# Performance work log

Measured on AMD Instinct MI355X. Metric: run time of the kernel, lower is better.

Reference implementation:

```python
import jax, jax.numpy as jnp
import numpy as np

TAU_PRE = 2.0
TAU_POST = 2.0


def setup_inputs() -> dict:
    key = jax.random.key(0)
    k1, k2, k3 = jax.random.split(key, 3)
    T, B, PRE, POST = 64, 16, 4096, 4096
    in_spikes = jax.random.uniform(k1, (T, B, PRE), dtype=jnp.float32)
    out_spikes = jax.random.uniform(k2, (T, B, POST), dtype=jnp.float32)
    weight = jax.random.normal(k3, (POST, PRE), dtype=jnp.float32)
    return {"in_spikes": in_spikes, "out_spikes": out_spikes, "weight": weight}


def reference(in_spikes, out_spikes, weight):
    # in_spikes: [T, B, pre]; out_spikes: [T, B, post]; weight: [post, pre]
    T, B, PRE = in_spikes.shape
    POST = out_spikes.shape[-1]

    def step(carry, xs):
        trace_pre, trace_post, delta_w = carry
        i_sp, o_sp = xs
        trace_pre = jnp.clip(trace_pre - trace_pre / TAU_PRE + i_sp, 0.0, 1.0)  # [B, pre]
        trace_post = trace_post - trace_post / TAU_POST + o_sp  # [B, post]
        # sum_b o[b,post]*trace_pre[b,pre] - (sum_b o[b,post]*trace_post[b,post]) * w[post,pre]
        dw = (jnp.einsum('bo,bp->op', o_sp, trace_pre)
              - (o_sp * trace_post).sum(0)[:, None] * weight)
        return (trace_pre, trace_post, delta_w + dw), None

    init = (jnp.zeros((B, PRE), in_spikes.dtype),
            jnp.zeros((B, POST), out_spikes.dtype),
            jnp.zeros((POST, PRE), weight.dtype))
    (trace_pre, trace_post, delta_w), _ = jax.lax.scan(step, init, (in_spikes, out_spikes))
    return delta_w
```

## Files before the change

### kernel.cpp

```cpp
#include <hip/hip_runtime.h>


#define T_STEPS 64
#define B_SZ    16
#define PRE     4096
#define POST    4096
#define K_TOT   1024

typedef __attribute__((ext_vector_type(8))) unsigned short ushort8;
typedef __attribute__((ext_vector_type(8))) __bf16 bf16x8;
typedef __attribute__((ext_vector_type(4))) float floatx4;

__device__ __forceinline__ unsigned short f2bf(float f) {
    unsigned int u = __float_as_uint(f);
    u += 0x7fff + ((u >> 16) & 1);
    return (unsigned short)(u >> 16);
}

__device__ __forceinline__ void glds16(const void* g, void* l) {
    __builtin_amdgcn_global_load_lds((const __attribute__((address_space(1))) void*)g,
                                     (__attribute__((address_space(3))) void*)l,
                                     16, 0, 0);
}

__global__ __launch_bounds__(256) void trace_convert(
        const float* __restrict__ in_spikes,
        const float* __restrict__ out_spikes,
        unsigned short* __restrict__ AT,
        unsigned short* __restrict__ BT,
        float* __restrict__ coef) {
    __shared__ float ldsf[4096];
    __shared__ unsigned short ot[128 * 34];
    __shared__ float cbuf[8][33];
    const int tid  = threadIdx.x;
    const int wave = tid >> 6;
    const int lane = tid & 63;
    const bool isA = blockIdx.x >= 128;
    const int p0 = (blockIdx.x & 127) * 32;
    const float* src = isA ? out_spikes : in_spikes;
    unsigned short* dst = isA ? AT : BT;

    const int bA = tid >> 5;
    const int pA = tid & 31;

    float st0 = 0.f, st1 = 0.f, c0 = 0.f, c1 = 0.f;

    for (int tc = 0; tc < 8; ++tc) {
        const int T0 = tc * 8;
        #pragma unroll
        for (int i = 0; i < 4; ++i) {
            const int q  = (wave * 4 + i) * 64 + lane;
            const int p  = (q & 7) * 4;
            const int b  = (q >> 3) & 15;
            const int tl = q >> 7;
            const float* g = src + ((size_t)((T0 + tl) * 16 + b)) * 4096 + p0 + p;
            glds16(g, (char*)ldsf + (size_t)(wave * 4 + i) * 1024);
        }
        __syncthreads();

        #pragma unroll
        for (int tl = 0; tl < 8; ++tl) {
            const float x0 = ldsf[tl * 512 + bA * 32 + pA];
            const float x1 = ldsf[tl * 512 + (bA + 8) * 32 + pA];
            if (isA) {
                st0 = 0.5f * st0 + x0; c0 += x0 * st0;
                st1 = 0.5f * st1 + x1; c1 += x1 * st1;
                ot[(tl * 16 + bA)     * 34 + pA] = f2bf(x0);
                ot[(tl * 16 + bA + 8) * 34 + pA] = f2bf(x1);
            } else {
                st0 = fminf(fmaxf(0.5f * st0 + x0, 0.f), 1.f);
                st1 = fminf(fmaxf(0.5f * st1 + x1, 0.f), 1.f);
                ot[(tl * 16 + bA)     * 34 + pA] = f2bf(st0);
                ot[(tl * 16 + bA + 8) * 34 + pA] = f2bf(st1);
            }
        }
        __syncthreads();

        const int pf = tid >> 3;
        const int c8 = tid & 7;
        #pragma unroll
        for (int i = 0; i < 2; ++i) {
            const int ch = c8 + i * 8;
            ushort8 v;
            #pragma unroll
            for (int s = 0; s < 8; ++s) v[s] = ot[(ch * 8 + s) * 34 + pf];
            *(ushort8*)&dst[(size_t)(p0 + pf) * K_TOT + T0 * 16 + ch * 8] = v;
        }
    }

    if (isA) {
        cbuf[bA][pA] = c0 + c1;
        __syncthreads();
        if (tid < 32) {
            float s = 0.f;
            #pragma unroll
            for (int r = 0; r < 8; ++r) s += cbuf[r][tid];
            coef[p0 + tid] = s;
        }
    }
}

#define NTILES 16

#define LOFF(buf, isB, kh) ((buf) * 65536 + (isB) * 32768 + (kh) * 16384)

__global__ __launch_bounds__(512, 2) void stdp_gemm_mfma(
        const unsigned short* __restrict__ AT,
        const unsigned short* __restrict__ BT,
        const float* __restrict__ W,
        const float* __restrict__ coef,
        float* __restrict__ Cout) {
    __shared__ __align__(16) char ldsraw[131072];

    const int tid  = threadIdx.x;
    const int lane = tid & 63;
    const int wave = tid >> 6;

    const int bid = blockIdx.x;
    const int f   = (bid & 7) * 32 + (bid >> 3);
    const int m0  = (f >> 4) * 256;
    const int n0  = (f & 15) * 256;

    const int wm  = (wave >> 2) * 128;
    const int wn  = (wave & 3) * 64;
    const int rml = lane & 15;
    const int q   = lane >> 4;
    const int swz16 = ((q ^ ((rml >> 1) & 3)) << 4);

    floatx4 acc[8][4];
    #pragma unroll
    for (int i = 0; i < 8; ++i)
        #pragma unroll
        for (int j = 0; j < 4; ++j)
            acc[i][j] = (floatx4){0.f, 0.f, 0.f, 0.f};
    bf16x8 bv[4];

    const int cid0 = wave * 64 + lane;
    const int row0 = cid0 >> 2;
    const int g0   = (cid0 & 3) ^ ((row0 >> 1) & 3);
    const unsigned short* gA0 = AT + (size_t)(m0 + row0) * K_TOT + g0 * 8;
    const unsigned short* gB0 = BT + (size_t)(n0 + row0) * K_TOT + g0 * 8;

    #define STG(isB, t, kh)                                                        \
        do {                                                                       \
            const unsigned short* s0_ = ((isB) ? gB0 : gA0) + (t) * 64 + (kh) * 32;\
            char* d_ = ldsraw + LOFF((t) & 1, (isB), (kh)) + wave * 1024;          \
            glds16(s0_, d_);                                                       \
            glds16(s0_ + (size_t)128 * K_TOT, d_ + 8192);                          \
        } while (0)

    #define PHASE(bufc, khc, mqc, SISB, ST, SKH, SCOND, WM)                        \
        do {                                                                       \
            const char* Ab_ = ldsraw + LOFF(bufc, 0, khc);                         \
            const char* Bb_ = ldsraw + LOFF(bufc, 1, khc);                         \
            if ((mqc) == 0) {                                                      \
                _Pragma("unroll")                                                  \
                for (int ni = 0; ni < 4; ++ni)                                     \
                    bv[ni] = *(const bf16x8*)(Bb_ + (wn + ni * 16 + rml) * 64 + swz16); \
            }                                                                      \
            bf16x8 af_[4];                                                         \
            _Pragma("unroll")                                                      \
            for (int k4 = 0; k4 < 4; ++k4)                                         \
                af_[k4] = *(const bf16x8*)(Ab_ + (wm + (mqc) * 64 + k4 * 16 + rml) * 64 + swz16); \
            if (SCOND) STG(SISB, ST, SKH);                                         \
            if ((WM) == 1)      asm volatile("s_waitcnt vmcnt(4)" ::: "memory");   \
            else if ((WM) == 2) asm volatile("s_waitcnt vmcnt(0)" ::: "memory");   \
            __builtin_amdgcn_s_barrier();                                          \
            __builtin_amdgcn_sched_barrier(0);                                     \
            __builtin_amdgcn_s_setprio(1);                                         \
            _Pragma("unroll")                                                      \
            for (int k4 = 0; k4 < 4; ++k4)                                         \
                _Pragma("unroll")                                                  \
                for (int ni = 0; ni < 4; ++ni)                                     \
                    acc[(mqc) * 4 + k4][ni] = __builtin_amdgcn_mfma_f32_16x16x32_bf16( \
                        af_[k4], bv[ni], acc[(mqc) * 4 + k4][ni], 0, 0, 0);        \
            __builtin_amdgcn_s_setprio(0);                                         \
            __builtin_amdgcn_s_barrier();                                          \
            __builtin_amdgcn_sched_barrier(0);                                     \
        } while (0)

    STG(0, 0, 0); STG(1, 0, 0); STG(0, 0, 1); STG(1, 0, 1);
    STG(0, 1, 0); STG(1, 1, 0); STG(0, 1, 1); STG(1, 1, 1);
    asm volatile("s_waitcnt vmcnt(8)" ::: "memory");
    __builtin_amdgcn_s_barrier();
    __builtin_amdgcn_sched_barrier(0);

    for (int i = 0; i < 8; ++i) {
        const int t2 = 2 * i + 2, t3 = 2 * i + 3, tA = 2 * i + 1;
        const int wm4 = (i < 7) ? 1 : 2;
        const int wm8 = (i < 7) ? 1 : 0;
        PHASE(0, 0, 0, 0, tA, 1, i > 0,      0);
        PHASE(0, 0, 1, 1, tA, 1, i > 0,      0);
        PHASE(0, 1, 0, 0, t2, 0, t2 < NTILES, 0);
        PHASE(0, 1, 1, 1, t2, 0, t2 < NTILES, wm4);
        PHASE(1, 0, 0, 0, t2, 1, t2 < NTILES, 0);
        PHASE(1, 0, 1, 1, t2, 1, t2 < NTILES, 0);
        PHASE(1, 1, 0, 0, t3, 0, t3 < NTILES, 0);
        PHASE(1, 1, 1, 1, t3, 0, t3 < NTILES, wm8);
    }

    const int colp = n0 + wn + rml;
    const int q4   = lane >> 4;
    #pragma unroll
    for (int mi = 0; mi < 8; ++mi) {
        #pragma unroll
        for (int r = 0; r < 4; ++r) {
            const int o = m0 + wm + mi * 16 + q4 * 4 + r;
            const float cf = coef[o];
            const float* wrow = &W[(size_t)o * PRE + colp];
            float* crow = &Cout[(size_t)o * PRE + colp];
            #pragma unroll
            for (int ni = 0; ni < 4; ++ni)
                crow[ni * 16] = acc[mi][ni][r] - cf * wrow[ni * 16];
        }
    }
    #undef PHASE
    #undef STG
}

extern "C" void kernel_launch(void* const* d_in, const int* in_sizes, int n_in,
                              void* d_out, int out_size, void* d_ws, size_t ws_size,
                              hipStream_t stream) {
    const float* in_spikes  = (const float*)d_in[0];
    const float* out_spikes = (const float*)d_in[1];
    const float* weight     = (const float*)d_in[2];
    float* out = (float*)d_out;

    unsigned short* AT = (unsigned short*)d_ws;
    unsigned short* BT = AT + (size_t)POST * K_TOT;
    float* coef = (float*)(BT + (size_t)PRE * K_TOT);

    trace_convert<<<256, 256, 0, stream>>>(in_spikes, out_spikes, AT, BT, coef);

    stdp_gemm_mfma<<<256, 512, 0, stream>>>(AT, BT, weight, coef, out);
}
```

Baseline: 180.8 us.

## Rewrite trace_convert with register-prefetched loads and more, smaller blocks

The trace/convert prepass now uses 512 blocks of 16 columns instead of 256 blocks of 32. Each thread keeps one running trace and loads its inputs directly into registers, double-buffering the next 8 timesteps while it processes the current 8. This replaces the global_load_lds staging and halves LDS use, and the __syncthreads calls become raw s_barriers. The aim is to shorten the memory-bound prepass by hiding load latency and using more CUs. The cost is 64-byte column reads per row, which may coalesce worse.

```diff
diff --git a/kernel.cpp b/kernel.cpp
--- a/kernel.cpp
+++ b/kernel.cpp
@@ -29,79 +29,77 @@
         unsigned short* __restrict__ AT,
         unsigned short* __restrict__ BT,
         float* __restrict__ coef) {
-    __shared__ float ldsf[4096];
-    __shared__ unsigned short ot[128 * 34];
-    __shared__ float cbuf[8][33];
+    __shared__ unsigned short ot[128 * 17];
+    __shared__ float cbuf[16 * 17];
     const int tid  = threadIdx.x;
-    const int wave = tid >> 6;
-    const int lane = tid & 63;
-    const bool isA = blockIdx.x >= 128;
-    const int p0 = (blockIdx.x & 127) * 32;
+    const bool isA = blockIdx.x >= 256;
+    const int p0 = (blockIdx.x & 255) * 16;
     const float* src = isA ? out_spikes : in_spikes;
     unsigned short* dst = isA ? AT : BT;
 
-    const int bA = tid >> 5;
-    const int pA = tid & 31;
-
-    float st0 = 0.f, st1 = 0.f, c0 = 0.f, c1 = 0.f;
-
-    for (int tc = 0; tc < 8; ++tc) {
-        const int T0 = tc * 8;
-        #pragma unroll
-        for (int i = 0; i < 4; ++i) {
-            const int q  = (wave * 4 + i) * 64 + lane;
-            const int p  = (q & 7) * 4;
-            const int b  = (q >> 3) & 15;
-            const int tl = q >> 7;
-            const float* g = src + ((size_t)((T0 + tl) * 16 + b)) * 4096 + p0 + p;
-            glds16(g, (char*)ldsf + (size_t)(wave * 4 + i) * 1024);
-        }
-        __syncthreads();
-
+    const int p = tid & 15;
+    const int b = tid >> 4;
+    const float* gbase = src + (size_t)b * PRE + p0 + p;
+
+    const int pf = tid >> 4;
+    const int ch = tid & 15;
+    unsigned short* dstf = &dst[(size_t)(p0 + pf) * K_TOT + ch * 8];
+
+    float x[2][8];
+    float st = 0.f, c0 = 0.f;
+
+    #pragma unroll
+    for (int tl = 0; tl < 8; ++tl) x[0][tl] = gbase[(size_t)tl * 65536];
+
+    #pragma unroll
+    for (int c = 0; c < 8; ++c) {
+        if (c < 7) {
+            #pragma unroll
+            for (int tl = 0; tl < 8; ++tl)
+                x[(c + 1) & 1][tl] = gbase[(size_t)((c + 1) * 8 + tl) * 65536];
+        }
         #pragma unroll
         for (int tl = 0; tl < 8; ++tl) {
-            const float x0 = ldsf[tl * 512 + bA * 32 + pA];
-            const float x1 = ldsf[tl * 512 + (bA + 8) * 32 + pA];
+            const float xv = x[c & 1][tl];
+            unsigned short ov;
             if (isA) {
-                st0 = 0.5f * st0 + x0; c0 += x0 * st0;
-                st1 = 0.5f * st1 + x1; c1 += x1 * st1;
-                ot[(tl * 16 + bA)     * 34 + pA] = f2bf(x0);
-                ot[(tl * 16 + bA + 8) * 34 + pA] = f2bf(x1);
+                st = 0.5f * st + xv;
+                c0 += xv * st;
+                ov = f2bf(xv);
             } else {
-                st0 = fminf(fmaxf(0.5f * st0 + x0, 0.f), 1.f);
-                st1 = fminf(fmaxf(0.5f * st1 + x1, 0.f), 1.f);
-                ot[(tl * 16 + bA)     * 34 + pA] = f2bf(st0);
-                ot[(tl * 16 + bA + 8) * 34 + pA] = f2bf(st1);
+                st = fminf(fmaxf(0.5f * st + xv, 0.f), 1.f);
+                ov = f2bf(st);
             }
-        }
-        __syncthreads();
-
-        const int pf = tid >> 3;
-        const int c8 = tid & 7;
-        #pragma unroll
-        for (int i = 0; i < 2; ++i) {
-            const int ch = c8 + i * 8;
-            ushort8 v;
-            #pragma unroll
-            for (int s = 0; s < 8; ++s) v[s] = ot[(ch * 8 + s) * 34 + pf];
-            *(ushort8*)&dst[(size_t)(p0 + pf) * K_TOT + T0 * 16 + ch * 8] = v;
-        }
+            ot[(tl * 16 + b) * 17 + p] = ov;
+        }
+        asm volatile("s_waitcnt lgkmcnt(0)" ::: "memory");
+        __builtin_amdgcn_s_barrier();
+        __builtin_amdgcn_sched_barrier(0);
+
+        ushort8 v;
+        #pragma unroll
+        for (int s = 0; s < 8; ++s) v[s] = ot[(ch * 8 + s) * 17 + pf];
+        *(ushort8*)&dstf[c * 128] = v;
+
+        asm volatile("s_waitcnt lgkmcnt(0)" ::: "memory");
+        __builtin_amdgcn_s_barrier();
+        __builtin_amdgcn_sched_barrier(0);
     }
 
     if (isA) {
-        cbuf[bA][pA] = c0 + c1;
-        __syncthreads();
-        if (tid < 32) {
+        cbuf[b * 17 + p] = c0;
+        asm volatile("s_waitcnt lgkmcnt(0)" ::: "memory");
+        __builtin_amdgcn_s_barrier();
+        if (tid < 16) {
             float s = 0.f;
             #pragma unroll
-            for (int r = 0; r < 8; ++r) s += cbuf[r][tid];
+            for (int r = 0; r < 16; ++r) s += cbuf[r * 17 + tid];
             coef[p0 + tid] = s;
         }
     }
 }
 
 #define NTILES 16
-
 #define LOFF(buf, isB, kh) ((buf) * 65536 + (isB) * 32768 + (kh) * 16384)
 
 __global__ __launch_bounds__(512, 2) void stdp_gemm_mfma(
@@ -230,7 +228,8 @@
     unsigned short* BT = AT + (size_t)POST * K_TOT;
     float* coef = (float*)(BT + (size_t)PRE * K_TOT);
 
-    trace_convert<<<256, 256, 0, stream>>>(in_spikes, out_spikes, AT, BT, coef);
-
-    stdp_gemm_mfma<<<256, 512, 0, stream>>>(AT, BT, weight, coef, out);
-}
+    trace_convert<<<512, 256, 0, stream>>>(in_spikes, out_spikes, AT, BT, coef);
+
+    dim3 grid(256);
+    stdp_gemm_mfma<<<grid, 512, 0, stream>>>(AT, BT, weight, coef, out);
+}
```

New measurement: 181.8 us. Within noise of the previous version (+0.5%).
